# Optimization experiments

Measured on AMD Instinct MI355X. Metric: run time of the kernel, lower is better.

The kernel has to match this reference:

```python
import jax, jax.numpy as jnp
import numpy as np

IN_, OUT_, HID, B = 1024, 1024, 4, 8192

def setup_inputs() -> dict:
    key = jax.random.key(0)
    k_x, k_w1, k_b1, k_w2, k_b2 = jax.random.split(key, 5)
    x = jax.random.normal(k_x, (B, IN_), dtype=jnp.float32)
    # Stacked params for out_ tiny MLPs: Linear(in,4) -> LeakyReLU(0.1) -> Linear(4,1)
    s1 = 1.0 / np.sqrt(IN_)
    s2 = 1.0 / np.sqrt(HID)
    W1 = jax.random.uniform(k_w1, (OUT_, IN_, HID), dtype=jnp.float32, minval=-s1, maxval=s1)
    b1 = jax.random.uniform(k_b1, (OUT_, HID), dtype=jnp.float32, minval=-s1, maxval=s1)
    W2 = jax.random.uniform(k_w2, (OUT_, HID), dtype=jnp.float32, minval=-s2, maxval=s2)
    b2 = jax.random.uniform(k_b2, (OUT_,), dtype=jnp.float32, minval=-s2, maxval=s2)
    return {"x": x, "W1": W1, "b1": b1, "W2": W2, "b2": b2}

def reference(x, W1, b1, W2, b2):
    # h[b,o,h] = x[b,:] @ W1[o] + b1[o]  (shared input across all out_ MLPs)
    h = jnp.einsum('bi,oih->boh', x, W1) + b1
    h = jnp.where(h >= 0, h, 0.1 * h)  # LeakyReLU(0.1)
    # out[b,o] = h[b,o,:] @ W2[o] + b2[o]; equals torch.cat of per-MLP scalars
    out = jnp.einsum('boh,oh->bo', h, W2) + b2
    return out
```

## Files before the change

kernel.cpp:

```cpp
#include <hip/hip_runtime.h>
#include <hip/hip_bf16.h>

#define IN_DIM  1024
#define OUT_DIM 1024
#define HID     4
#define BATCH   8192
#define NCOL    (OUT_DIM * HID)

typedef __bf16 bf16x8 __attribute__((ext_vector_type(8)));
typedef float  f32x4  __attribute__((ext_vector_type(4)));

__device__ __forceinline__ unsigned short f2bf(float f) {
  union { float f; unsigned int u; } v; v.f = f;
  unsigned int u = v.u;
  u += 0x7FFFu + ((u >> 16) & 1u);
  return (unsigned short)(u >> 16);
}

__global__ __launch_bounds__(256) void cvt_xg_kernel(const float* __restrict__ x,
                                                     uint4* __restrict__ xg) {
  int g = blockIdx.x * 256 + threadIdx.x;
  int bl = g & 15, ko = (g >> 4) & 127, c4 = g >> 11;
  const float4* xp = (const float4*)(x + (size_t)(c4 * 16 + bl) * 1024 + ko * 8);
  float4 v0 = xp[0], v1 = xp[1];
  uint4 r;
  r.x = f2bf(v0.x) | ((unsigned)f2bf(v0.y) << 16);
  r.y = f2bf(v0.z) | ((unsigned)f2bf(v0.w) << 16);
  r.z = f2bf(v1.x) | ((unsigned)f2bf(v1.y) << 16);
  r.w = f2bf(v1.z) | ((unsigned)f2bf(v1.w) << 16);
  xg[g] = r;
}

__global__ __launch_bounds__(256) void cvt_w1t_kernel(const float* __restrict__ W1,
                                                      ushort4* __restrict__ out) {
  int b = blockIdx.x;
  int g = ((b & 7) * ((int)gridDim.x >> 3) + (b >> 3)) * 256 + threadIdx.x;
  int i4 = g & 255;
  int oh = g >> 8;
  int h = oh & 3, o = oh >> 2;
  const float* src = W1 + (size_t)o * 4096 + h;
  ushort4 r;
  r.x = f2bf(src[(i4 * 4 + 0) * 4]);
  r.y = f2bf(src[(i4 * 4 + 1) * 4]);
  r.z = f2bf(src[(i4 * 4 + 2) * 4]);
  r.w = f2bf(src[(i4 * 4 + 3) * 4]);
  out[(size_t)oh * 256 + i4] = r;
}

__device__ __forceinline__ void gload16(const void* g, void* l) {
  __builtin_amdgcn_global_load_lds(
      (const __attribute__((address_space(1))) unsigned int*)g,
      (__attribute__((address_space(3))) unsigned int*)l, 16, 0, 0);
}

__global__ __launch_bounds__(256, 2) void mlp_gemm_kernel(
    const unsigned short* __restrict__ A,
    const unsigned short* __restrict__ Bg,
    const f32x4* __restrict__ b1v,
    const f32x4* __restrict__ w2v,
    const float* __restrict__ b2,
    float* __restrict__ out) {
  __shared__ __align__(16) unsigned short lds[32768];

  const int bid = blockIdx.x;
  const int xcd = bid & 7, loc = bid >> 3;
  const int bn = xcd * 8 + (loc & 7);
  const int bm = loc >> 3;
  const int tileM = bm * 256, tileN = bn * 128;

  const int t = threadIdx.x;
  const int lane = t & 63, wid = t >> 6;
  const int wm = wid >> 1, wn = wid & 1;
  const int frow = lane & 15, jq = lane >> 4;

  const int sr8 = t >> 3, slt = t & 7;
  const int scol = ((slt ^ (sr8 & 7)) << 3);
  const unsigned short* Asrc = A + (size_t)(tileM + sr8) * IN_DIM + scol;

  auto stage = [&](int kt, int p) {
    const int kb = kt * 64;
    unsigned short* lA = lds + p * 16384 + t * 8;
#pragma unroll
    for (int i = 0; i < 8; ++i)
      gload16(Asrc + (size_t)(32 * i) * IN_DIM + kb, lA + i * 2048);
  };

  const int c40 = (tileN >> 4) + wn * 4;
  const char* xgb = (const char*)Bg;
  const char* bp0 = xgb + ((size_t)(c40 * 128 + jq) * 16 + frow) * 16;
  const char* bp1 = bp0 + 32768;
  const char* bp2 = bp0 + 65536;
  const char* bp3 = bp0 + 98304;

  f32x4 acc[8][4];
#pragma unroll
  for (int m = 0; m < 8; ++m)
#pragma unroll
    for (int n = 0; n < 4; ++n) acc[m][n] = f32x4{0.f, 0.f, 0.f, 0.f};

  const int pk0 = (jq ^ (frow & 7)) << 3;
  const int aRow = (wm * 128 + frow) * 64;

  bf16x8 b0[4], b1_[4];
  stage(0, 0);
  b0[0] = *(const bf16x8*)(bp0);  b1_[0] = *(const bf16x8*)(bp0 + 1024);
  b0[1] = *(const bf16x8*)(bp1);  b1_[1] = *(const bf16x8*)(bp1 + 1024);
  b0[2] = *(const bf16x8*)(bp2);  b1_[2] = *(const bf16x8*)(bp2 + 1024);
  b0[3] = *(const bf16x8*)(bp3);  b1_[3] = *(const bf16x8*)(bp3 + 1024);
  bp0 += 2048; bp1 += 2048; bp2 += 2048; bp3 += 2048;
  asm volatile("s_waitcnt vmcnt(0)" ::: "memory");
  __builtin_amdgcn_s_barrier();

  for (int kt = 0; kt < 16; ++kt) {
    const int cur = kt & 1;
    if (kt < 15) stage(kt + 1, cur ^ 1);

    const unsigned short* aB = lds + cur * 16384 + aRow;
    bf16x8 a[8];
#pragma unroll
    for (int mf = 0; mf < 8; ++mf)
      a[mf] = *(const bf16x8*)(aB + mf * 1024 + pk0);
#pragma unroll
    for (int mf = 0; mf < 8; ++mf) {
      acc[mf][0] = __builtin_amdgcn_mfma_f32_16x16x32_bf16(a[mf], b0[0], acc[mf][0], 0, 0, 0);
      acc[mf][1] = __builtin_amdgcn_mfma_f32_16x16x32_bf16(a[mf], b0[1], acc[mf][1], 0, 0, 0);
      acc[mf][2] = __builtin_amdgcn_mfma_f32_16x16x32_bf16(a[mf], b0[2], acc[mf][2], 0, 0, 0);
      acc[mf][3] = __builtin_amdgcn_mfma_f32_16x16x32_bf16(a[mf], b0[3], acc[mf][3], 0, 0, 0);
    }
#pragma unroll
    for (int mf = 0; mf < 8; ++mf)
      a[mf] = *(const bf16x8*)(aB + mf * 1024 + (pk0 ^ 32));
#pragma unroll
    for (int mf = 0; mf < 8; ++mf) {
      acc[mf][0] = __builtin_amdgcn_mfma_f32_16x16x32_bf16(a[mf], b1_[0], acc[mf][0], 0, 0, 0);
      acc[mf][1] = __builtin_amdgcn_mfma_f32_16x16x32_bf16(a[mf], b1_[1], acc[mf][1], 0, 0, 0);
      acc[mf][2] = __builtin_amdgcn_mfma_f32_16x16x32_bf16(a[mf], b1_[2], acc[mf][2], 0, 0, 0);
      acc[mf][3] = __builtin_amdgcn_mfma_f32_16x16x32_bf16(a[mf], b1_[3], acc[mf][3], 0, 0, 0);
    }

    if (kt < 15) {
      asm volatile("s_waitcnt vmcnt(0)" ::: "memory");
      b0[0] = *(const bf16x8*)(bp0);  b1_[0] = *(const bf16x8*)(bp0 + 1024);
      b0[1] = *(const bf16x8*)(bp1);  b1_[1] = *(const bf16x8*)(bp1 + 1024);
      b0[2] = *(const bf16x8*)(bp2);  b1_[2] = *(const bf16x8*)(bp2 + 1024);
      b0[3] = *(const bf16x8*)(bp3);  b1_[3] = *(const bf16x8*)(bp3 + 1024);
      bp0 += 2048; bp1 += 2048; bp2 += 2048; bp3 += 2048;
      __builtin_amdgcn_s_barrier();
    }
  }
  __syncthreads();

  float* LE = (float*)lds;
  const int obase = tileM >> 2;
#pragma unroll
  for (int mf = 0; mf < 8; ++mf) {
    int o_loc = wm * 32 + mf * 4 + jq;
    f32x4 b1q = b1v[obase + o_loc];
    f32x4 w2q = w2v[obase + o_loc];
#pragma unroll
    for (int nf = 0; nf < 4; ++nf) {
      int bat = wn * 64 + nf * 16 + frow;
      float v = 0.f;
#pragma unroll
      for (int h = 0; h < 4; ++h) {
        float hj = acc[mf][nf][h] + b1q[h];
        hj = (hj >= 0.f) ? hj : 0.1f * hj;
        v += hj * w2q[h];
      }
      LE[bat * 65 + o_loc] = v;
    }
  }
  __syncthreads();

  const int col = t & 63, rowb = t >> 6;
  const float b2s = b2[obase + col];
  float* outB = out + (size_t)tileN * OUT_DIM + obase;
#pragma unroll
  for (int i = 0; i < 32; ++i) {
    int row = rowb + i * 4;
    outB[(size_t)row * OUT_DIM + col] = LE[row * 65 + col] + b2s;
  }
}

__global__ __launch_bounds__(256) void fallback_kernel(
    const float* __restrict__ x, const float* __restrict__ W1,
    const float* __restrict__ b1, const float* __restrict__ W2,
    const float* __restrict__ b2, float* __restrict__ out) {
  int idx = blockIdx.x * 256 + threadIdx.x;
  if (idx >= BATCH * OUT_DIM) return;
  int bb = idx >> 10, o = idx & 1023;
  const float4* w1p = (const float4*)(W1 + (size_t)o * 4096);
  const float*  xp  = x + (size_t)bb * 1024;
  float4 acc = *(const float4*)(b1 + o * 4);
  for (int i = 0; i < 1024; ++i) {
    float xv = xp[i];
    float4 w = w1p[i];
    acc.x += xv * w.x; acc.y += xv * w.y; acc.z += xv * w.z; acc.w += xv * w.w;
  }
  float4 w2 = *(const float4*)(W2 + o * 4);
  float r = b2[o];
  r += ((acc.x >= 0.f) ? acc.x : 0.1f * acc.x) * w2.x;
  r += ((acc.y >= 0.f) ? acc.y : 0.1f * acc.y) * w2.y;
  r += ((acc.z >= 0.f) ? acc.z : 0.1f * acc.z) * w2.z;
  r += ((acc.w >= 0.f) ? acc.w : 0.1f * acc.w) * w2.w;
  out[(size_t)bb * OUT_DIM + o] = r;
}

extern "C" void kernel_launch(void* const* d_in, const int* in_sizes, int n_in,
                              void* d_out, int out_size, void* d_ws, size_t ws_size,
                              hipStream_t stream) {
  const float* x  = (const float*)d_in[0];
  const float* W1 = (const float*)d_in[1];
  const float* b1 = (const float*)d_in[2];
  const float* W2 = (const float*)d_in[3];
  const float* b2 = (const float*)d_in[4];
  float* out = (float*)d_out;

  size_t need = (size_t)BATCH * IN_DIM * 2 + (size_t)NCOL * IN_DIM * 2;
  if (ws_size >= need) {
    unsigned short* xg  = (unsigned short*)d_ws;
    unsigned short* w1t = xg + (size_t)BATCH * IN_DIM;
    cvt_xg_kernel<<<(BATCH * IN_DIM / 8) / 256, 256, 0, stream>>>(x, (uint4*)xg);
    cvt_w1t_kernel<<<(NCOL * IN_DIM / 4) / 256, 256, 0, stream>>>(W1, (ushort4*)w1t);
    mlp_gemm_kernel<<<(NCOL / 256) * (BATCH / 128), 256, 0, stream>>>(
        w1t, xg, (const f32x4*)b1, (const f32x4*)W2, b2, out);
  } else {
    fallback_kernel<<<(BATCH * OUT_DIM + 255) / 256, 256, 0, stream>>>(x, W1, b1, W2, b2, out);
  }
}
```

Measured before the change: 84.33 us.

## Double-buffer B fragments in registers and interleave LDS reads with MFMA chunks

Adds a second register buffer for the B fragments so the global loads for step k+1 are issued together with the LDS stage at the start of step k. The partial `s_waitcnt vmcnt(8)` waits only for the LDS-bound A loads, so the B loads can stay in flight during compute. The main loop is manually unrolled by two to ping-pong the buffers. A-fragment LDS reads are split into four-fragment chunks, with s_setprio around each MFMA group and sched_barriers to pin the schedule. This is meant to hide the B-load latency that the old vmcnt(0)-then-load sequence exposed, at the cost of more VGPRs, which could pressure occupancy at 2 blocks per CU.

```diff
diff --git a/kernel.cpp b/kernel.cpp
--- a/kernel.cpp
+++ b/kernel.cpp
@@ -86,11 +86,7 @@
   };
 
   const int c40 = (tileN >> 4) + wn * 4;
-  const char* xgb = (const char*)Bg;
-  const char* bp0 = xgb + ((size_t)(c40 * 128 + jq) * 16 + frow) * 16;
-  const char* bp1 = bp0 + 32768;
-  const char* bp2 = bp0 + 65536;
-  const char* bp3 = bp0 + 98304;
+  const char* bpB = (const char*)Bg + (((size_t)c40 * 128 + jq) * 16 + frow) * 16;
 
   f32x4 acc[8][4];
 #pragma unroll
@@ -101,50 +97,93 @@
   const int pk0 = (jq ^ (frow & 7)) << 3;
   const int aRow = (wm * 128 + frow) * 64;
 
-  bf16x8 b0[4], b1_[4];
+#define LOADB(dst, kt_) do {                                                   \
+    _Pragma("unroll")                                                          \
+    for (int nf_ = 0; nf_ < 4; ++nf_) {                                        \
+      dst[nf_ * 2 + 0] = *(const bf16x8*)(bpB + nf_ * 32768 + (kt_) * 2048);   \
+      dst[nf_ * 2 + 1] = *(const bf16x8*)(bpB + nf_ * 32768 + (kt_) * 2048 + 1024); \
+    } } while (0)
+
+#define COMPUTE_KT(cur_, BF) do {                                              \
+    const unsigned short* aB_ = lds + (cur_) * 16384 + aRow;                   \
+    bf16x8 a_[4];                                                              \
+    _Pragma("unroll")                                                          \
+    for (int i_ = 0; i_ < 4; ++i_) a_[i_] = *(const bf16x8*)(aB_ + i_ * 1024 + pk0); \
+    __builtin_amdgcn_s_setprio(1);                                             \
+    _Pragma("unroll")                                                          \
+    for (int mf_ = 0; mf_ < 4; ++mf_) {                                        \
+      acc[mf_][0] = __builtin_amdgcn_mfma_f32_16x16x32_bf16(a_[mf_], BF[0], acc[mf_][0], 0, 0, 0); \
+      acc[mf_][1] = __builtin_amdgcn_mfma_f32_16x16x32_bf16(a_[mf_], BF[2], acc[mf_][1], 0, 0, 0); \
+      acc[mf_][2] = __builtin_amdgcn_mfma_f32_16x16x32_bf16(a_[mf_], BF[4], acc[mf_][2], 0, 0, 0); \
+      acc[mf_][3] = __builtin_amdgcn_mfma_f32_16x16x32_bf16(a_[mf_], BF[6], acc[mf_][3], 0, 0, 0); \
+    }                                                                          \
+    __builtin_amdgcn_s_setprio(0);                                             \
+    _Pragma("unroll")                                                          \
+    for (int i_ = 0; i_ < 4; ++i_) a_[i_] = *(const bf16x8*)(aB_ + (4 + i_) * 1024 + pk0); \
+    __builtin_amdgcn_s_setprio(1);                                             \
+    _Pragma("unroll")                                                          \
+    for (int mf_ = 0; mf_ < 4; ++mf_) {                                        \
+      acc[4 + mf_][0] = __builtin_amdgcn_mfma_f32_16x16x32_bf16(a_[mf_], BF[0], acc[4 + mf_][0], 0, 0, 0); \
+      acc[4 + mf_][1] = __builtin_amdgcn_mfma_f32_16x16x32_bf16(a_[mf_], BF[2], acc[4 + mf_][1], 0, 0, 0); \
+      acc[4 + mf_][2] = __builtin_amdgcn_mfma_f32_16x16x32_bf16(a_[mf_], BF[4], acc[4 + mf_][2], 0, 0, 0); \
+      acc[4 + mf_][3] = __builtin_amdgcn_mfma_f32_16x16x32_bf16(a_[mf_], BF[6], acc[4 + mf_][3], 0, 0, 0); \
+    }                                                                          \
+    __builtin_amdgcn_s_setprio(0);                                             \
+    _Pragma("unroll")                                                          \
+    for (int i_ = 0; i_ < 4; ++i_) a_[i_] = *(const bf16x8*)(aB_ + i_ * 1024 + (pk0 ^ 32)); \
+    __builtin_amdgcn_s_setprio(1);                                             \
+    _Pragma("unroll")                                                          \
+    for (int mf_ = 0; mf_ < 4; ++mf_) {                                        \
+      acc[mf_][0] = __builtin_amdgcn_mfma_f32_16x16x32_bf16(a_[mf_], BF[1], acc[mf_][0], 0, 0, 0); \
+      acc[mf_][1] = __builtin_amdgcn_mfma_f32_16x16x32_bf16(a_[mf_], BF[3], acc[mf_][1], 0, 0, 0); \
+      acc[mf_][2] = __builtin_amdgcn_mfma_f32_16x16x32_bf16(a_[mf_], BF[5], acc[mf_][2], 0, 0, 0); \
+      acc[mf_][3] = __builtin_amdgcn_mfma_f32_16x16x32_bf16(a_[mf_], BF[7], acc[mf_][3], 0, 0, 0); \
+    }                                                                          \
+    __builtin_amdgcn_s_setprio(0);                                             \
+    _Pragma("unroll")                                                          \
+    for (int i_ = 0; i_ < 4; ++i_) a_[i_] = *(const bf16x8*)(aB_ + (4 + i_) * 1024 + (pk0 ^ 32)); \
+    __builtin_amdgcn_s_setprio(1);                                             \
+    _Pragma("unroll")                                                          \
+    for (int mf_ = 0; mf_ < 4; ++mf_) {                                        \
+      acc[4 + mf_][0] = __builtin_amdgcn_mfma_f32_16x16x32_bf16(a_[mf_], BF[1], acc[4 + mf_][0], 0, 0, 0); \
+      acc[4 + mf_][1] = __builtin_amdgcn_mfma_f32_16x16x32_bf16(a_[mf_], BF[3], acc[4 + mf_][1], 0, 0, 0); \
+      acc[4 + mf_][2] = __builtin_amdgcn_mfma_f32_16x16x32_bf16(a_[mf_], BF[5], acc[4 + mf_][2], 0, 0, 0); \
+      acc[4 + mf_][3] = __builtin_amdgcn_mfma_f32_16x16x32_bf16(a_[mf_], BF[7], acc[4 + mf_][3], 0, 0, 0); \
+    }                                                                          \
+    __builtin_amdgcn_s_setprio(0);                                             \
+  } while (0)
+
+  bf16x8 bA[8], bB[8];
+
   stage(0, 0);
-  b0[0] = *(const bf16x8*)(bp0);  b1_[0] = *(const bf16x8*)(bp0 + 1024);
-  b0[1] = *(const bf16x8*)(bp1);  b1_[1] = *(const bf16x8*)(bp1 + 1024);
-  b0[2] = *(const bf16x8*)(bp2);  b1_[2] = *(const bf16x8*)(bp2 + 1024);
-  b0[3] = *(const bf16x8*)(bp3);  b1_[3] = *(const bf16x8*)(bp3 + 1024);
-  bp0 += 2048; bp1 += 2048; bp2 += 2048; bp3 += 2048;
-  asm volatile("s_waitcnt vmcnt(0)" ::: "memory");
+  __builtin_amdgcn_sched_barrier(0);
+  LOADB(bA, 0);
+  __builtin_amdgcn_sched_barrier(0);
+  asm volatile("s_waitcnt vmcnt(8)" ::: "memory");
   __builtin_amdgcn_s_barrier();
 
-  for (int kt = 0; kt < 16; ++kt) {
-    const int cur = kt & 1;
-    if (kt < 15) stage(kt + 1, cur ^ 1);
-
-    const unsigned short* aB = lds + cur * 16384 + aRow;
-    bf16x8 a[8];
-#pragma unroll
-    for (int mf = 0; mf < 8; ++mf)
-      a[mf] = *(const bf16x8*)(aB + mf * 1024 + pk0);
-#pragma unroll
-    for (int mf = 0; mf < 8; ++mf) {
-      acc[mf][0] = __builtin_amdgcn_mfma_f32_16x16x32_bf16(a[mf], b0[0], acc[mf][0], 0, 0, 0);
-      acc[mf][1] = __builtin_amdgcn_mfma_f32_16x16x32_bf16(a[mf], b0[1], acc[mf][1], 0, 0, 0);
-      acc[mf][2] = __builtin_amdgcn_mfma_f32_16x16x32_bf16(a[mf], b0[2], acc[mf][2], 0, 0, 0);
-      acc[mf][3] = __builtin_amdgcn_mfma_f32_16x16x32_bf16(a[mf], b0[3], acc[mf][3], 0, 0, 0);
+#pragma unroll 1
+  for (int g = 0; g < 16; g += 2) {
+    {
+      if (g < 15) {
+        stage(g + 1, 1);
+        __builtin_amdgcn_sched_barrier(0);
+        LOADB(bB, g + 1);
+        __builtin_amdgcn_sched_barrier(0);
+      }
+      COMPUTE_KT(0, bA);
+      if (g < 15) asm volatile("s_waitcnt vmcnt(8)" ::: "memory");
+      __builtin_amdgcn_s_barrier();
     }
-#pragma unroll
-    for (int mf = 0; mf < 8; ++mf)
-      a[mf] = *(const bf16x8*)(aB + mf * 1024 + (pk0 ^ 32));
-#pragma unroll
-    for (int mf = 0; mf < 8; ++mf) {
-      acc[mf][0] = __builtin_amdgcn_mfma_f32_16x16x32_bf16(a[mf], b1_[0], acc[mf][0], 0, 0, 0);
-      acc[mf][1] = __builtin_amdgcn_mfma_f32_16x16x32_bf16(a[mf], b1_[1], acc[mf][1], 0, 0, 0);
-      acc[mf][2] = __builtin_amdgcn_mfma_f32_16x16x32_bf16(a[mf], b1_[2], acc[mf][2], 0, 0, 0);
-      acc[mf][3] = __builtin_amdgcn_mfma_f32_16x16x32_bf16(a[mf], b1_[3], acc[mf][3], 0, 0, 0);
-    }
-
-    if (kt < 15) {
-      asm volatile("s_waitcnt vmcnt(0)" ::: "memory");
-      b0[0] = *(const bf16x8*)(bp0);  b1_[0] = *(const bf16x8*)(bp0 + 1024);
-      b0[1] = *(const bf16x8*)(bp1);  b1_[1] = *(const bf16x8*)(bp1 + 1024);
-      b0[2] = *(const bf16x8*)(bp2);  b1_[2] = *(const bf16x8*)(bp2 + 1024);
-      b0[3] = *(const bf16x8*)(bp3);  b1_[3] = *(const bf16x8*)(bp3 + 1024);
-      bp0 += 2048; bp1 += 2048; bp2 += 2048; bp3 += 2048;
+    {
+      if (g + 1 < 15) {
+        stage(g + 2, 0);
+        __builtin_amdgcn_sched_barrier(0);
+        LOADB(bA, g + 2);
+        __builtin_amdgcn_sched_barrier(0);
+      }
+      COMPUTE_KT(1, bB);
+      if (g + 1 < 15) asm volatile("s_waitcnt vmcnt(8)" ::: "memory");
       __builtin_amdgcn_s_barrier();
     }
   }
@@ -180,6 +219,8 @@
     int row = rowb + i * 4;
     outB[(size_t)row * OUT_DIM + col] = LE[row * 65 + col] + b2s;
   }
+#undef LOADB
+#undef COMPUTE_KT
 }
 
 __global__ __launch_bounds__(256) void fallback_kernel(
```

Result: slower. 144.6 us (+71.4%).

## Shrink GEMM tile to 128x128 with 1x4 warp layout for higher occupancy

Applied to the files above, without the earlier changes.

Halves the M tile from 256 to 128 weight columns, cuts LDS to 32KB, and reorganizes the four waves as a 1x4 split along the batch dimension, each owning 8x2 MFMA fragments. B fragments are now loaded directly at the start of each k-step instead of being prefetched a step ahead. Launch bounds go to 3 blocks per SM and the grid doubles. The aim is more resident blocks and better latency hiding, at the cost of lower arithmetic intensity per tile, more redundant global traffic for x, and exposed B-load latency inside the loop.

```diff
diff --git a/kernel.cpp b/kernel.cpp
--- a/kernel.cpp
+++ b/kernel.cpp
@@ -53,24 +53,23 @@
       (__attribute__((address_space(3))) unsigned int*)l, 16, 0, 0);
 }
 
-__global__ __launch_bounds__(256, 2) void mlp_gemm_kernel(
+__global__ __launch_bounds__(256, 3) void mlp_gemm_kernel(
     const unsigned short* __restrict__ A,
     const unsigned short* __restrict__ Bg,
     const f32x4* __restrict__ b1v,
     const f32x4* __restrict__ w2v,
     const float* __restrict__ b2,
     float* __restrict__ out) {
-  __shared__ __align__(16) unsigned short lds[32768];
+  __shared__ __align__(16) unsigned short lds[16384];
 
   const int bid = blockIdx.x;
   const int xcd = bid & 7, loc = bid >> 3;
   const int bn = xcd * 8 + (loc & 7);
   const int bm = loc >> 3;
-  const int tileM = bm * 256, tileN = bn * 128;
+  const int tileM = bm * 128, tileN = bn * 128;
 
   const int t = threadIdx.x;
-  const int lane = t & 63, wid = t >> 6;
-  const int wm = wid >> 1, wn = wid & 1;
+  const int lane = t & 63, wn = t >> 6;
   const int frow = lane & 15, jq = lane >> 4;
 
   const int sr8 = t >> 3, slt = t & 7;
@@ -79,35 +78,26 @@
 
   auto stage = [&](int kt, int p) {
     const int kb = kt * 64;
-    unsigned short* lA = lds + p * 16384 + t * 8;
-#pragma unroll
-    for (int i = 0; i < 8; ++i)
+    unsigned short* lA = lds + p * 8192 + t * 8;
+#pragma unroll
+    for (int i = 0; i < 4; ++i)
       gload16(Asrc + (size_t)(32 * i) * IN_DIM + kb, lA + i * 2048);
   };
 
-  const int c40 = (tileN >> 4) + wn * 4;
-  const char* xgb = (const char*)Bg;
-  const char* bp0 = xgb + ((size_t)(c40 * 128 + jq) * 16 + frow) * 16;
-  const char* bp1 = bp0 + 32768;
-  const char* bp2 = bp0 + 65536;
-  const char* bp3 = bp0 + 98304;
-
-  f32x4 acc[8][4];
-#pragma unroll
-  for (int m = 0; m < 8; ++m)
-#pragma unroll
-    for (int n = 0; n < 4; ++n) acc[m][n] = f32x4{0.f, 0.f, 0.f, 0.f};
+  const int c40 = (tileN >> 4) + wn * 2;
+  const char* bpB = (const char*)Bg + (((size_t)c40 * 128 + jq) * 16 + frow) * 16;
+
+  f32x4 acc[8][2];
+#pragma unroll
+  for (int m = 0; m < 8; ++m) {
+    acc[m][0] = f32x4{0.f, 0.f, 0.f, 0.f};
+    acc[m][1] = f32x4{0.f, 0.f, 0.f, 0.f};
+  }
 
   const int pk0 = (jq ^ (frow & 7)) << 3;
-  const int aRow = (wm * 128 + frow) * 64;
-
-  bf16x8 b0[4], b1_[4];
+  const int pk1 = pk0 ^ 32;
+
   stage(0, 0);
-  b0[0] = *(const bf16x8*)(bp0);  b1_[0] = *(const bf16x8*)(bp0 + 1024);
-  b0[1] = *(const bf16x8*)(bp1);  b1_[1] = *(const bf16x8*)(bp1 + 1024);
-  b0[2] = *(const bf16x8*)(bp2);  b1_[2] = *(const bf16x8*)(bp2 + 1024);
-  b0[3] = *(const bf16x8*)(bp3);  b1_[3] = *(const bf16x8*)(bp3 + 1024);
-  bp0 += 2048; bp1 += 2048; bp2 += 2048; bp3 += 2048;
   asm volatile("s_waitcnt vmcnt(0)" ::: "memory");
   __builtin_amdgcn_s_barrier();
 
@@ -115,36 +105,45 @@
     const int cur = kt & 1;
     if (kt < 15) stage(kt + 1, cur ^ 1);
 
-    const unsigned short* aB = lds + cur * 16384 + aRow;
-    bf16x8 a[8];
-#pragma unroll
-    for (int mf = 0; mf < 8; ++mf)
-      a[mf] = *(const bf16x8*)(aB + mf * 1024 + pk0);
-#pragma unroll
-    for (int mf = 0; mf < 8; ++mf) {
-      acc[mf][0] = __builtin_amdgcn_mfma_f32_16x16x32_bf16(a[mf], b0[0], acc[mf][0], 0, 0, 0);
-      acc[mf][1] = __builtin_amdgcn_mfma_f32_16x16x32_bf16(a[mf], b0[1], acc[mf][1], 0, 0, 0);
-      acc[mf][2] = __builtin_amdgcn_mfma_f32_16x16x32_bf16(a[mf], b0[2], acc[mf][2], 0, 0, 0);
-      acc[mf][3] = __builtin_amdgcn_mfma_f32_16x16x32_bf16(a[mf], b0[3], acc[mf][3], 0, 0, 0);
-    }
-#pragma unroll
-    for (int mf = 0; mf < 8; ++mf)
-      a[mf] = *(const bf16x8*)(aB + mf * 1024 + (pk0 ^ 32));
-#pragma unroll
-    for (int mf = 0; mf < 8; ++mf) {
-      acc[mf][0] = __builtin_amdgcn_mfma_f32_16x16x32_bf16(a[mf], b1_[0], acc[mf][0], 0, 0, 0);
-      acc[mf][1] = __builtin_amdgcn_mfma_f32_16x16x32_bf16(a[mf], b1_[1], acc[mf][1], 0, 0, 0);
-      acc[mf][2] = __builtin_amdgcn_mfma_f32_16x16x32_bf16(a[mf], b1_[2], acc[mf][2], 0, 0, 0);
-      acc[mf][3] = __builtin_amdgcn_mfma_f32_16x16x32_bf16(a[mf], b1_[3], acc[mf][3], 0, 0, 0);
+    const char* bk = bpB + kt * 2048;
+    bf16x8 b00 = *(const bf16x8*)(bk);
+    bf16x8 b01 = *(const bf16x8*)(bk + 1024);
+    bf16x8 b10 = *(const bf16x8*)(bk + 32768);
+    bf16x8 b11 = *(const bf16x8*)(bk + 32768 + 1024);
+
+    const unsigned short* aB = lds + cur * 8192 + frow * 64;
+    bf16x8 a[4];
+#pragma unroll
+    for (int i = 0; i < 4; ++i) a[i] = *(const bf16x8*)(aB + i * 1024 + pk0);
+#pragma unroll
+    for (int mf = 0; mf < 4; ++mf) {
+      acc[mf][0] = __builtin_amdgcn_mfma_f32_16x16x32_bf16(a[mf], b00, acc[mf][0], 0, 0, 0);
+      acc[mf][1] = __builtin_amdgcn_mfma_f32_16x16x32_bf16(a[mf], b10, acc[mf][1], 0, 0, 0);
+    }
+#pragma unroll
+    for (int i = 0; i < 4; ++i) a[i] = *(const bf16x8*)(aB + (4 + i) * 1024 + pk0);
+#pragma unroll
+    for (int mf = 0; mf < 4; ++mf) {
+      acc[4 + mf][0] = __builtin_amdgcn_mfma_f32_16x16x32_bf16(a[mf], b00, acc[4 + mf][0], 0, 0, 0);
+      acc[4 + mf][1] = __builtin_amdgcn_mfma_f32_16x16x32_bf16(a[mf], b10, acc[4 + mf][1], 0, 0, 0);
+    }
+#pragma unroll
+    for (int i = 0; i < 4; ++i) a[i] = *(const bf16x8*)(aB + i * 1024 + pk1);
+#pragma unroll
+    for (int mf = 0; mf < 4; ++mf) {
+      acc[mf][0] = __builtin_amdgcn_mfma_f32_16x16x32_bf16(a[mf], b01, acc[mf][0], 0, 0, 0);
+      acc[mf][1] = __builtin_amdgcn_mfma_f32_16x16x32_bf16(a[mf], b11, acc[mf][1], 0, 0, 0);
+    }
+#pragma unroll
+    for (int i = 0; i < 4; ++i) a[i] = *(const bf16x8*)(aB + (4 + i) * 1024 + pk1);
+#pragma unroll
+    for (int mf = 0; mf < 4; ++mf) {
+      acc[4 + mf][0] = __builtin_amdgcn_mfma_f32_16x16x32_bf16(a[mf], b01, acc[4 + mf][0], 0, 0, 0);
+      acc[4 + mf][1] = __builtin_amdgcn_mfma_f32_16x16x32_bf16(a[mf], b11, acc[4 + mf][1], 0, 0, 0);
     }
 
     if (kt < 15) {
       asm volatile("s_waitcnt vmcnt(0)" ::: "memory");
-      b0[0] = *(const bf16x8*)(bp0);  b1_[0] = *(const bf16x8*)(bp0 + 1024);
-      b0[1] = *(const bf16x8*)(bp1);  b1_[1] = *(const bf16x8*)(bp1 + 1024);
-      b0[2] = *(const bf16x8*)(bp2);  b1_[2] = *(const bf16x8*)(bp2 + 1024);
-      b0[3] = *(const bf16x8*)(bp3);  b1_[3] = *(const bf16x8*)(bp3 + 1024);
-      bp0 += 2048; bp1 += 2048; bp2 += 2048; bp3 += 2048;
       __builtin_amdgcn_s_barrier();
     }
   }
@@ -154,12 +153,12 @@
   const int obase = tileM >> 2;
 #pragma unroll
   for (int mf = 0; mf < 8; ++mf) {
-    int o_loc = wm * 32 + mf * 4 + jq;
+    int o_loc = mf * 4 + jq;
     f32x4 b1q = b1v[obase + o_loc];
     f32x4 w2q = w2v[obase + o_loc];
 #pragma unroll
-    for (int nf = 0; nf < 4; ++nf) {
-      int bat = wn * 64 + nf * 16 + frow;
+    for (int nf = 0; nf < 2; ++nf) {
+      int bat = wn * 32 + nf * 16 + frow;
       float v = 0.f;
 #pragma unroll
       for (int h = 0; h < 4; ++h) {
@@ -167,18 +166,18 @@
         hj = (hj >= 0.f) ? hj : 0.1f * hj;
         v += hj * w2q[h];
       }
-      LE[bat * 65 + o_loc] = v;
+      LE[bat * 33 + o_loc] = v;
     }
   }
   __syncthreads();
 
-  const int col = t & 63, rowb = t >> 6;
+  const int col = t & 31, rowb = t >> 5;
   const float b2s = b2[obase + col];
   float* outB = out + (size_t)tileN * OUT_DIM + obase;
 #pragma unroll
-  for (int i = 0; i < 32; ++i) {
-    int row = rowb + i * 4;
-    outB[(size_t)row * OUT_DIM + col] = LE[row * 65 + col] + b2s;
+  for (int i = 0; i < 16; ++i) {
+    int row = rowb + i * 8;
+    outB[(size_t)row * OUT_DIM + col] = LE[row * 33 + col] + b2s;
   }
 }
 
@@ -222,7 +221,7 @@
     unsigned short* w1t = xg + (size_t)BATCH * IN_DIM;
     cvt_xg_kernel<<<(BATCH * IN_DIM / 8) / 256, 256, 0, stream>>>(x, (uint4*)xg);
     cvt_w1t_kernel<<<(NCOL * IN_DIM / 4) / 256, 256, 0, stream>>>(W1, (ushort4*)w1t);
-    mlp_gemm_kernel<<<(NCOL / 256) * (BATCH / 128), 256, 0, stream>>>(
+    mlp_gemm_kernel<<<(NCOL / 128) * (BATCH / 128), 256, 0, stream>>>(
         w1t, xg, (const f32x4*)b1, (const f32x4*)W2, b2, out);
   } else {
     fallback_kernel<<<(BATCH * OUT_DIM + 255) / 256, 256, 0, stream>>>(x, W1, b1, W2, b2, out);
```

Result: no change. 84.79 us (+0.6%).
